# Kernel tuning notes

Measured on AMD Instinct MI355X. Metric: run time of the kernel, lower is better.

## Reference

```python
import jax, jax.numpy as jnp
import numpy as np

N, E, D, H = 50000, 800000, 128, 8
HD = D // H
EPS = 1e-5


def _layernorm(x, w, b):
    # Custom LayerNorm from the repo: divides by (unbiased std + eps), not sqrt(var+eps)
    mu = x.mean(axis=-1, keepdims=True)
    sd = x.std(axis=-1, keepdims=True, ddof=1)
    return (x - mu) / (sd + EPS) * w + b


def setup_inputs() -> dict:
    key = jax.random.key(0)
    ks = jax.random.split(key, 16)
    s = 1.0 / np.sqrt(D)
    inp = {
        "feats": jax.random.normal(ks[0], (N, D), jnp.float32),
        "edge_index": jax.random.randint(ks[1], (E, 2), 0, N, jnp.int32),
        "Wq": jax.random.normal(ks[2], (D, D), jnp.float32) * s,
        "bq": jnp.zeros((D,), jnp.float32),
        "Wk": jax.random.normal(ks[3], (D, D), jnp.float32) * s,
        "bk": jnp.zeros((D,), jnp.float32),
        "Wv": jax.random.normal(ks[4], (D, D), jnp.float32) * s,
        "bv": jnp.zeros((D,), jnp.float32),
        "Wo": jax.random.normal(ks[5], (D, D), jnp.float32) * s,
        "bo": jnp.zeros((D,), jnp.float32),
        "ln1_w": jnp.ones((D,), jnp.float32),
        "ln1_b": jnp.zeros((D,), jnp.float32),
        "ln2_w": jnp.ones((D,), jnp.float32),
        "ln2_b": jnp.zeros((D,), jnp.float32),
        "W1": jax.random.normal(ks[6], (4 * D, D), jnp.float32) * s,
        "b1": jnp.zeros((4 * D,), jnp.float32),
        "W2": jax.random.normal(ks[7], (D, 4 * D), jnp.float32) * (1.0 / np.sqrt(4 * D)),
        "b2": jnp.zeros((D,), jnp.float32),
    }
    return inp


def reference(feats, edge_index, Wq, bq, Wk, bk, Wv, bv, Wo, bo,
              ln1_w, ln1_b, ln2_w, ln2_b, W1, b1, W2, b2):
    n = feats.shape[0]
    row, col = edge_index[:, 0], edge_index[:, 1]

    # --- multi-head dot-product attention over edges (dropout = identity, eval mode) ---
    x2 = _layernorm(feats, ln1_w, ln1_b)
    q = (x2 @ Wq.T + bq).reshape(n, H, HD)
    k = (x2 @ Wk.T + bk).reshape(n, H, HD)
    v = (x2 @ Wv.T + bv).reshape(n, H, HD)

    # per-edge scores: q[col] . k[row] / sqrt(head_dim)  -> [E, H]
    scores = jnp.einsum('ehd,ehd->eh', q[col], k[row]) / np.sqrt(HD).astype(np.float32)

    # scatter softmax normalized over groups of `row`
    smax = jax.ops.segment_max(scores, row, num_segments=n)       # [N, H]
    ex = jnp.exp(scores - smax[row])                              # [E, H]
    denom = jax.ops.segment_sum(ex, row, num_segments=n)         # [N, H]
    alpha = ex / denom[row]                                       # [E, H]

    # weighted messages, aggregated at col via scatter_add
    msg = alpha[:, :, None] * v[row]                              # [E, H, HD]
    agg = jax.ops.segment_sum(msg, col, num_segments=n).reshape(n, D)
    att = agg @ Wo.T + bo

    feats = feats + att  # residual 1

    # --- MLP block: note ReLU after BOTH linears (fc_dims=[4D, D], D != 1) ---
    x2 = _layernorm(feats, ln2_w, ln2_b)
    h = jax.nn.relu(x2 @ W1.T + b1)
    h = jax.nn.relu(h @ W2.T + b2)
    feats = feats + h  # residual 2
    return feats
```

## Files before the change

### kernel.cpp

```cpp
#include <hip/hip_runtime.h>
#include <hip/hip_bf16.h>
#include <math.h>

#define H_HEADS 8
constexpr float LN_EPS = 1e-5f;
constexpr int NBCH = 64;
constexpr int NSEG = 4;

using short8 = __attribute__((ext_vector_type(8))) short;
using f32x4  = __attribute__((ext_vector_type(4))) float;
using f32x2  = __attribute__((ext_vector_type(2))) float;
using half2v = __attribute__((ext_vector_type(2))) _Float16;

#if defined(__has_builtin)
#  if __has_builtin(__builtin_amdgcn_cvt_pk_f32_fp8) && __has_builtin(__builtin_amdgcn_cvt_pk_fp8_f32)
#    define HAS_CVT_FP8 1
#  endif
#endif
#ifndef HAS_CVT_FP8
#  define HAS_CVT_FP8 0
#endif

__device__ __forceinline__ ushort f2bf(float v){
  __hip_bfloat16 h = __float2bfloat16(v);
  return *reinterpret_cast<ushort*>(&h);
}
__device__ __forceinline__ float bf2f(ushort u){
  return __uint_as_float(((unsigned)u) << 16);
}

__device__ __forceinline__ unsigned char f32_to_fp8(float v){
#if HAS_CVT_FP8
  return (unsigned char)(__builtin_amdgcn_cvt_pk_fp8_f32(v, v, 0, false) & 0xff);
#else
  _Float16 hv = (_Float16)v;
  ushort h = __builtin_bit_cast(ushort, hv);
  unsigned sign = (h >> 8) & 0x80;
  unsigned p = h & 0x7fff;
  if (p < 0x2400u) return (unsigned char)sign;
  unsigned q = (p - 0x2000u + 0x40u) >> 7;
  if (q > 0x7eu) q = 0x7eu;
  return (unsigned char)(sign | q);
#endif
}
__device__ __forceinline__ float fp8_to_f32(unsigned b){
  unsigned p = b & 0x7f;
  ushort hbits = (ushort)(((b & 0x80) << 8) | (p ? ((p << 7) + 0x2000u) : 0));
  _Float16 hv = __builtin_bit_cast(_Float16, hbits);
  return (float)hv;
}

__device__ __forceinline__ void stage16(const ushort* g, ushort* l){
  __builtin_amdgcn_global_load_lds((const __attribute__((address_space(1))) unsigned*)g,
                                   (__attribute__((address_space(3))) unsigned*)l,
                                   16, 0, 0);
}

struct CvtArgs { const float* s[6]; ushort* d[6]; int cnt[6]; };
__global__ void cvt6_kernel(CvtArgs a){
  int w = blockIdx.y;
  int i = blockIdx.x*blockDim.x + threadIdx.x;
  if (i < a.cnt[w]) a.d[w][i] = f2bf(a.s[w][i]);
}

template<int K, int RELU, int RESID, int OUTMODE>
__device__ __forceinline__ void gemm_lds_body(
    const ushort* __restrict__ A, const ushort* __restrict__ W,
    const float* __restrict__ bias, const float* __restrict__ resid,
    void* __restrict__ out, int M, int Nout, int cb, ushort* Wl){
  constexpr int NCH = K / 128;
  int t = threadIdx.x;
  int wid = t >> 6, lane = t & 63;
  int mb = blockIdx.x * 128 + wid * 16;
  int lrow = lane & 15, kgrp = lane >> 4;
  int row = mb + lrow;
  bool waveok = mb < M;
  bool rowok = row < M;
  const ushort* arow = A + (size_t)(rowok ? row : (M-1)) * K + kgrp*8;

  f32x4 acc[8] = {};
  short8 af[2][4];

  #pragma unroll
  for (int p = 0; p < 4; ++p){
    int L = p*512 + t;
    int colp = L >> 4, sp = L & 15;
    stage16(W + (size_t)colp*K + ((sp ^ (colp & 7)) << 3),
            (ushort*)((char*)Wl + ((size_t)(p*512 + (t & ~63)))*16));
  }
  if (waveok){
    #pragma unroll
    for (int kk = 0; kk < 4; ++kk)
      af[0][kk] = *(const short8*)(arow + kk*32);
  }

  #pragma unroll
  for (int ci = 0; ci < NCH; ++ci){
    __syncthreads();
    int cur = ci & 1;
    if (waveok){
      if (ci + 1 < NCH){
        #pragma unroll
        for (int kk = 0; kk < 4; ++kk)
          af[cur^1][kk] = *(const short8*)(arow + (ci+1)*128 + kk*32);
      }
      #pragma unroll
      for (int kk = 0; kk < 4; ++kk){
        #pragma unroll
        for (int nt = 0; nt < 8; ++nt){
          int colc = nt*16 + lrow;
          int g = kk*4 + kgrp;
          short8 bfv = *(const short8*)((const char*)Wl + colc*256 + ((g ^ (colc & 7))*16));
          acc[nt] = __builtin_amdgcn_mfma_f32_16x16x32_bf16(af[cur][kk], bfv, acc[nt], 0, 0, 0);
        }
      }
    }
    if (ci + 1 < NCH){
      __syncthreads();
      const ushort* Wc = W + (ci+1)*128;
      #pragma unroll
      for (int p = 0; p < 4; ++p){
        int L = p*512 + t;
        int colp = L >> 4, sp = L & 15;
        stage16(Wc + (size_t)colp*K + ((sp ^ (colp & 7)) << 3),
                (ushort*)((char*)Wl + ((size_t)(p*512 + (t & ~63)))*16));
      }
    }
  }
  if (!waveok) return;

  int r0 = mb + kgrp*4;
  #pragma unroll
  for (int nt = 0; nt < 8; ++nt){
    int c = cb + nt*16 + lrow;
    float bsum = bias[c];
    #pragma unroll
    for (int i = 0; i < 4; ++i){
      int r = r0 + i;
      if (r >= M) continue;
      float v = acc[nt][i] + bsum;
      if (RELU)  v = fmaxf(v, 0.0f);
      if (RESID) v += resid[(size_t)r*Nout + c];
      if (OUTMODE == 1) ((ushort*)out)[(size_t)r*Nout + c] = f2bf(v);
      else if (OUTMODE == 2){
        _Float16 hv = (_Float16)v;
        ((ushort*)out)[(size_t)r*Nout + c] = __builtin_bit_cast(ushort, hv);
      } else ((float*)out)[(size_t)r*Nout + c] = v;
    }
  }
}

template<int K, int RELU, int RESID, int OUTMODE>
__global__ __launch_bounds__(512) void gemm_lds(
    const ushort* __restrict__ A, const ushort* __restrict__ Wfull,
    const float* __restrict__ bias, const float* __restrict__ resid,
    void* __restrict__ out, int M, int Nout){
  __shared__ __align__(16) ushort Wl[16384];
  int cb = blockIdx.y * 128;
  gemm_lds_body<K,RELU,RESID,OUTMODE>(A, Wfull + (size_t)cb*K, bias, resid, out, M, Nout, cb, Wl);
}

__global__ __launch_bounds__(512) void qkv_fused(
    const float* __restrict__ feats, const ushort* __restrict__ Wcat,
    const float* __restrict__ ln1w, const float* __restrict__ ln1b,
    const float* __restrict__ bq, const float* __restrict__ bk, const float* __restrict__ bv,
    unsigned char* __restrict__ qb8, ushort* __restrict__ kb, ushort* __restrict__ vb, int M){
  constexpr int K = 128;
  __shared__ __align__(16) ushort Wl[16384];
  int t = threadIdx.x;
  int wid = t >> 6, lane = t & 63;
  int mb = blockIdx.x * 128 + wid * 16;
  int lrow = lane & 15, kgrp = lane >> 4;
  int row = mb + lrow;
  bool waveok = mb < M;
  bool rowok = row < M;
  int rclamp = rowok ? row : (M-1);
  const float* frow = feats + (size_t)rclamp*K + kgrp*8;

  float fx[32];
  #pragma unroll
  for (int kk = 0; kk < 4; ++kk){
    float4 a = *(const float4*)(frow + kk*32);
    float4 b = *(const float4*)(frow + kk*32 + 4);
    fx[kk*8+0]=a.x; fx[kk*8+1]=a.y; fx[kk*8+2]=a.z; fx[kk*8+3]=a.w;
    fx[kk*8+4]=b.x; fx[kk*8+5]=b.y; fx[kk*8+6]=b.z; fx[kk*8+7]=b.w;
  }
  float s = 0.f;
  #pragma unroll
  for (int i = 0; i < 32; ++i) s += fx[i];
  s += __shfl_xor(s, 16); s += __shfl_xor(s, 32);
  float mu = s * (1.0f/128.0f);
  float ss = 0.f;
  #pragma unroll
  for (int i = 0; i < 32; ++i){ fx[i] -= mu; ss += fx[i]*fx[i]; }
  ss += __shfl_xor(ss, 16); ss += __shfl_xor(ss, 32);
  float inv = 1.0f / (sqrtf(ss * (1.0f/127.0f)) + LN_EPS);

  short8 af[4];
  #pragma unroll
  for (int kk = 0; kk < 4; ++kk){
    const float* wp = ln1w + kgrp*8 + kk*32;
    const float* bp = ln1b + kgrp*8 + kk*32;
    float4 w0 = *(const float4*)wp,  w1 = *(const float4*)(wp+4);
    float4 b0 = *(const float4*)bp,  b1 = *(const float4*)(bp+4);
    float wv[8] = {w0.x,w0.y,w0.z,w0.w,w1.x,w1.y,w1.z,w1.w};
    float bvv[8]= {b0.x,b0.y,b0.z,b0.w,b1.x,b1.y,b1.z,b1.w};
    #pragma unroll
    for (int j = 0; j < 8; ++j)
      af[kk][j] = (short)f2bf(fx[kk*8+j]*inv*wv[j] + bvv[j]);
  }

  #pragma unroll
  for (int y = 0; y < 3; ++y){
    if (y) __syncthreads();
    const ushort* W = Wcat + (size_t)y*16384;
    #pragma unroll
    for (int p = 0; p < 4; ++p){
      int L = p*512 + t;
      int colp = L >> 4, sp = L & 15;
      stage16(W + (size_t)colp*K + ((sp ^ (colp & 7)) << 3),
              (ushort*)((char*)Wl + ((size_t)(p*512 + (t & ~63)))*16));
    }
    __syncthreads();
    if (waveok){
      const float* bias = (y==0) ? bq : (y==1) ? bk : bv;
      f32x4 acc[8] = {};
      #pragma unroll
      for (int kk = 0; kk < 4; ++kk){
        #pragma unroll
        for (int nt = 0; nt < 8; ++nt){
          int colc = nt*16 + lrow;
          int g = kk*4 + kgrp;
          short8 bfv = *(const short8*)((const char*)Wl + colc*256 + ((g ^ (colc & 7))*16));
          acc[nt] = __builtin_amdgcn_mfma_f32_16x16x32_bf16(af[kk], bfv, acc[nt], 0, 0, 0);
        }
      }
      int r0 = mb + kgrp*4;
      #pragma unroll
      for (int nt = 0; nt < 8; ++nt){
        int c = nt*16 + lrow;
        float bsum = bias[c];
        #pragma unroll
        for (int i = 0; i < 4; ++i){
          int r = r0 + i;
          if (r >= M) continue;
          float v = acc[nt][i] + bsum;
          if (y == 0)      qb8[(size_t)r*128 + c] = f32_to_fp8(v);
          else if (y == 1){
            _Float16 hv = (_Float16)v;
            kb[(size_t)r*128 + c] = __builtin_bit_cast(ushort, hv);
          } else           vb[(size_t)r*128 + c] = f2bf(v);
        }
      }
    }
  }
}

__global__ __launch_bounds__(512) void gemm_wo_ln2(
    const ushort* __restrict__ A, const ushort* __restrict__ W,
    const float* __restrict__ bias, const float* __restrict__ feats,
    const float* __restrict__ lnw, const float* __restrict__ lnb,
    float* __restrict__ outp, ushort* __restrict__ x2b, int M){
  constexpr int K = 128;
  __shared__ __align__(16) ushort Wl[16384];
  int t = threadIdx.x;
  int wid = t >> 6, lane = t & 63;
  int mb = blockIdx.x * 128 + wid * 16;
  int lrow = lane & 15, kgrp = lane >> 4;
  int row = mb + lrow;
  bool waveok = mb < M;
  bool rowok = row < M;
  const ushort* arow = A + (size_t)(rowok ? row : (M-1)) * K + kgrp*8;

  f32x4 acc[8] = {};
  short8 af[4];

  #pragma unroll
  for (int p = 0; p < 4; ++p){
    int L = p*512 + t;
    int colp = L >> 4, sp = L & 15;
    stage16(W + (size_t)colp*K + ((sp ^ (colp & 7)) << 3),
            (ushort*)((char*)Wl + ((size_t)(p*512 + (t & ~63)))*16));
  }
  if (waveok){
    #pragma unroll
    for (int kk = 0; kk < 4; ++kk)
      af[kk] = *(const short8*)(arow + kk*32);
  }
  __syncthreads();
  if (!waveok) return;

  #pragma unroll
  for (int kk = 0; kk < 4; ++kk){
    #pragma unroll
    for (int nt = 0; nt < 8; ++nt){
      int colc = nt*16 + lrow;
      int g = kk*4 + kgrp;
      short8 bfv = *(const short8*)((const char*)Wl + colc*256 + ((g ^ (colc & 7))*16));
      acc[nt] = __builtin_amdgcn_mfma_f32_16x16x32_bf16(af[kk], bfv, acc[nt], 0, 0, 0);
    }
  }

  int r0 = mb + kgrp*4;
  float vv[8][4];
  float lw[8], lb[8];
  #pragma unroll
  for (int nt = 0; nt < 8; ++nt){
    int c = nt*16 + lrow;
    float bsum = bias[c];
    lw[nt] = lnw[c]; lb[nt] = lnb[c];
    #pragma unroll
    for (int i = 0; i < 4; ++i){
      int r = r0 + i;
      float v = 0.f;
      if (r < M){
        v = acc[nt][i] + bsum + feats[(size_t)r*128 + c];
        outp[(size_t)r*128 + c] = v;
      }
      vv[nt][i] = v;
    }
  }
  #pragma unroll
  for (int i = 0; i < 4; ++i){
    int r = r0 + i;
    float s = 0.f;
    #pragma unroll
    for (int nt = 0; nt < 8; ++nt) s += vv[nt][i];
    #pragma unroll
    for (int o = 1; o < 16; o <<= 1) s += __shfl_xor(s, o);
    float mu = s * (1.0f/128.0f);
    float ss = 0.f;
    float d[8];
    #pragma unroll
    for (int nt = 0; nt < 8; ++nt){ d[nt] = vv[nt][i] - mu; ss += d[nt]*d[nt]; }
    #pragma unroll
    for (int o = 1; o < 16; o <<= 1) ss += __shfl_xor(ss, o);
    float sd = sqrtf(ss * (1.0f/127.0f));
    float inv = 1.0f / (sd + LN_EPS);
    if (r < M){
      #pragma unroll
      for (int nt = 0; nt < 8; ++nt){
        int c = nt*16 + lrow;
        x2b[(size_t)r*128 + c] = f2bf(d[nt]*inv*lw[nt] + lb[nt]);
      }
    }
  }
}

__global__ __launch_bounds__(256) void hist_seg2(const int* __restrict__ ei,
    unsigned* __restrict__ copies, int E, int n, int nw, int chunk, int nsb){
  __shared__ unsigned hh[12544];
  int b = blockIdx.x, s = blockIdx.y, t = threadIdx.x;
  int bin0 = s * nsb;
  int bin1 = min(bin0 + nsb, n);
  int words = (bin1 - bin0 + 1) >> 1;
  for (int i = t; i < 2*words; i += 256) hh[i] = 0;
  __syncthreads();
  int lo = b*chunk, hi = min(lo + chunk, E);
  for (int e = lo + t; e < hi; e += 256){
    int2 rc = ((const int2*)ei)[e];
    if (rc.x >= bin0 && rc.x < bin1)
      atomicAdd(&hh[(rc.x - bin0) >> 1], 1u << ((rc.x & 1)*16));
    if (rc.y >= bin0 && rc.y < bin1)
      atomicAdd(&hh[words + ((rc.y - bin0) >> 1)], 1u << ((rc.y & 1)*16));
  }
  __syncthreads();
  unsigned* d0 = copies + (size_t)b*nw + (bin0 >> 1);
  unsigned* d1 = copies + (size_t)(NBCH + b)*nw + (bin0 >> 1);
  for (int i = t; i < words; i += 256){ d0[i] = hh[i]; d1[i] = hh[words + i]; }
}

__global__ __launch_bounds__(256) void scan_fold2(const unsigned* __restrict__ copies,
    int* __restrict__ cnt2, ushort* __restrict__ choff, int* __restrict__ partial,
    int n, int nw, int npb){
  int y = blockIdx.y;
  int t = threadIdx.x;
  int bin = blockIdx.x*256 + t;
  int run = 0;
  if (bin < n){
    const unsigned* cp = copies + (size_t)y*NBCH*nw + (bin >> 1);
    int sh = (bin & 1)*16;
    for (int b = 0; b < NBCH; ++b){
      int c = (int)((cp[(size_t)b*nw] >> sh) & 0xffffu);
      choff[((size_t)y*NBCH + b)*n + bin] = (ushort)run;
      run += c;
    }
    cnt2[(size_t)y*n + bin] = run;
  }
  __shared__ int sm[256];
  sm[t] = (bin < n) ? run : 0;
  __syncthreads();
  for (int off = 128; off; off >>= 1){
    if (t < off) sm[t] += sm[t+off];
    __syncthreads();
  }
  if (t == 0) partial[y*npb + blockIdx.x] = sm[0];
}

__global__ __launch_bounds__(256) void scan_mid(int* __restrict__ partial, int nb,
                                                int* __restrict__ rptr, int* __restrict__ cptr, int n){
  int y = blockIdx.y;
  int* p = partial + y*nb;
  int t = threadIdx.x;
  __shared__ int sm[256];
  sm[t] = (t < nb) ? p[t] : 0;
  __syncthreads();
  for (int off = 1; off < 256; off <<= 1){
    int v = (t >= off) ? sm[t-off] : 0;
    __syncthreads();
    sm[t] += v;
    __syncthreads();
  }
  if (t < nb) p[t] = (t == 0) ? 0 : sm[t-1];
  if (t == 0) (y ? cptr : rptr)[n] = sm[255];
}

__global__ __launch_bounds__(256) void scan_scatter2(const int* __restrict__ cnt2,
    const int* __restrict__ partial, int* __restrict__ rptr, int* __restrict__ cptr,
    int n, int npb){
  int y = blockIdx.y;
  int* ptr = y ? cptr : rptr;
  int t = threadIdx.x;
  int bin = blockIdx.x*256 + t;
  int v = (bin < n) ? cnt2[(size_t)y*n + bin] : 0;
  __shared__ int sm[256];
  sm[t] = v;
  __syncthreads();
  for (int off = 1; off < 256; off <<= 1){
    int x = (t >= off) ? sm[t-off] : 0;
    __syncthreads();
    sm[t] += x;
    __syncthreads();
  }
  if (bin < n) ptr[bin] = partial[y*npb + blockIdx.x] + sm[t] - v;
}

__global__ __launch_bounds__(256) void fill_r_seg(const int* __restrict__ ei,
    const int* __restrict__ rptr, const ushort* __restrict__ choffR,
    int* __restrict__ rcol, int* __restrict__ pose, int E, int n, int chunk, int nsb){
  __shared__ unsigned hh[8192];
  int b = blockIdx.x, s = blockIdx.y, t = threadIdx.x;
  int bin0 = s * nsb;
  int bin1 = min(bin0 + nsb, n);
  int words = (bin1 - bin0 + 1) >> 1;
  for (int i = t; i < words; i += 256) hh[i] = 0;
  __syncthreads();
  const ushort* chb = choffR + (size_t)b*n;
  int lo = b*chunk, hi = min(lo + chunk, E);
  for (int e = lo + t; e < hi; e += 256){
    int2 rc = ((const int2*)ei)[e];
    int bin = rc.x;
    if (bin < bin0 || bin >= bin1) continue;
    int sh = (bin & 1)*16;
    unsigned old = atomicAdd(&hh[(bin - bin0) >> 1], 1u << sh);
    int rank = (int)((old >> sh) & 0xffffu);
    int pos = rptr[bin] + (int)chb[bin] + rank;
    rcol[pos] = rc.y;
    pose[e] = pos;
  }
}

__global__ __launch_bounds__(256) void fill_c_seg(const int* __restrict__ ei,
    const int* __restrict__ cptr, const ushort* __restrict__ choffC,
    const int* __restrict__ pose, int* __restrict__ crow, int* __restrict__ cposr,
    int E, int n, int chunk, int nsb){
  __shared__ unsigned hh[8192];
  int b = blockIdx.x, s = blockIdx.y, t = threadIdx.x;
  int bin0 = s * nsb;
  int bin1 = min(bin0 + nsb, n);
  int words = (bin1 - bin0 + 1) >> 1;
  for (int i = t; i < words; i += 256) hh[i] = 0;
  __syncthreads();
  const ushort* chb = choffC + (size_t)b*n;
  int lo = b*chunk, hi = min(lo + chunk, E);
  for (int e = lo + t; e < hi; e += 256){
    int2 rc = ((const int2*)ei)[e];
    int bin = rc.y;
    if (bin < bin0 || bin >= bin1) continue;
    int sh = (bin & 1)*16;
    unsigned old = atomicAdd(&hh[(bin - bin0) >> 1], 1u << sh);
    int rank = (int)((old >> sh) & 0xffffu);
    int pos = cptr[bin] + (int)chb[bin] + rank;
    crow[pos] = rc.x;
    cposr[pose[e]] = pos;
  }
}

__device__ __forceinline__ float qdot16q8(const unsigned char* __restrict__ qb8, int c, int h,
                                          const float* kf){
  const uint4* qp = (const uint4*)(qb8 + (size_t)c*128 + h*16);
  uint4 q = *qp;
  unsigned w[4] = {q.x, q.y, q.z, q.w};
  float s = 0.f;
  #pragma unroll
  for (int i = 0; i < 4; ++i){
#if HAS_CVT_FP8
    f32x2 lo = __builtin_amdgcn_cvt_pk_f32_fp8(w[i], false);
    f32x2 hi = __builtin_amdgcn_cvt_pk_f32_fp8(w[i], true);
    s = fmaf(lo[0], kf[4*i+0], s);
    s = fmaf(lo[1], kf[4*i+1], s);
    s = fmaf(hi[0], kf[4*i+2], s);
    s = fmaf(hi[1], kf[4*i+3], s);
#else
    #pragma unroll
    for (int j = 0; j < 4; ++j)
      s = fmaf(fp8_to_f32((w[i] >> (8*j)) & 0xffu), kf[4*i+j], s);
#endif
  }
  return s * 0.25f;
}

template<int NS>
__device__ __forceinline__ void softmax_rows(const unsigned char* __restrict__ qb8,
    const int* __restrict__ rcol, const int* __restrict__ cposr,
    ushort* __restrict__ cbuf, const float* kf, int lo, int hi, int h, int el,
    int rl, int cpl){
  float sreg[NS];
  float m = -1e30f;
  #pragma unroll
  for (int ts = 0; ts < NS; ++ts){
    int c = __shfl(rl, el + ts*8);
    int j = lo + el + ts*8;
    float s = -1e30f;
    if (j < hi) s = qdot16q8(qb8, c, h, kf);
    sreg[ts] = s;
    m = fmaxf(m, s);
  }
  if (NS == 8)
    for (int j = lo + el + 64; j < hi; j += 8)
      m = fmaxf(m, qdot16q8(qb8, rcol[j], h, kf));
  #pragma unroll
  for (int o = 8; o < 64; o <<= 1) m = fmaxf(m, __shfl_xor(m, o));

  float d = 0.f;
  #pragma unroll
  for (int ts = 0; ts < NS; ++ts){
    int j = lo + el + ts*8;
    if (j < hi){ float e = __expf(sreg[ts] - m); sreg[ts] = e; d += e; }
  }
  if (NS == 8)
    for (int j = lo + el + 64; j < hi; j += 8)
      d += __expf(qdot16q8(qb8, rcol[j], h, kf) - m);
  #pragma unroll
  for (int o = 8; o < 64; o <<= 1) d += __shfl_xor(d, o);
  float invd = 1.0f / d;

  #pragma unroll
  for (int ts = 0; ts < NS; ++ts){
    int cp = __shfl(cpl, el + ts*8);
    int j = lo + el + ts*8;
    if (j < hi) cbuf[(size_t)cp*8 + h] = f2bf(sreg[ts] * invd);
  }
  if (NS == 8)
    for (int j = lo + el + 64; j < hi; j += 8){
      float s = qdot16q8(qb8, rcol[j], h, kf);
      cbuf[(size_t)cposr[j]*8 + h] = f2bf(__expf(s - m) * invd);
    }
}

__global__ void row_softmax_kernel(const unsigned char* __restrict__ qb8,
                                   const ushort* __restrict__ kb,
                                   const int* __restrict__ rptr, const int* __restrict__ rcol,
                                   const int* __restrict__ cposr,
                                   ushort* __restrict__ cbuf, int n){
  int wid = threadIdx.x >> 6, lane = threadIdx.x & 63;
  int r = blockIdx.x * (blockDim.x >> 6) + wid;
  if (r >= n) return;
  int lo = rptr[r], hi = rptr[r+1];
  if (lo >= hi) return;
  int h = lane & 7, el = lane >> 3;

  int jl = lo + lane;
  bool jok = jl < hi;
  int rl  = rcol [jok ? jl : lo];
  int cpl = cposr[jok ? jl : lo];

  float kf[16];
  {
    const int4* kp = (const int4*)(kb + (size_t)r*128 + h*16);
    int4 k0 = kp[0], k1 = kp[1];
    int kw[8] = {k0.x,k0.y,k0.z,k0.w,k1.x,k1.y,k1.z,k1.w};
    #pragma unroll
    for (int i = 0; i < 8; ++i){
      half2v k2 = __builtin_bit_cast(half2v, kw[i]);
      kf[2*i]   = (float)k2.x;
      kf[2*i+1] = (float)k2.y;
    }
  }

  int deg = hi - lo;
  if (deg <= 16)      softmax_rows<2>(qb8, rcol, cposr, cbuf, kf, lo, hi, h, el, rl, cpl);
  else if (deg <= 32) softmax_rows<4>(qb8, rcol, cposr, cbuf, kf, lo, hi, h, el, rl, cpl);
  else                softmax_rows<8>(qb8, rcol, cposr, cbuf, kf, lo, hi, h, el, rl, cpl);
}

__global__ void agg_kernel(const ushort* __restrict__ vb, const ushort* __restrict__ cbuf,
                           const int* __restrict__ cptr, const int* __restrict__ crow,
                           ushort* __restrict__ aggb, int n){
  int wid = threadIdx.x >> 6, lane = threadIdx.x & 63;
  int node = blockIdx.x * (blockDim.x >> 6) + wid;
  if (node >= n) return;
  int lo = cptr[node], hi = cptr[node+1];
  int deg = hi - lo;
  int oct = lane >> 3, l8 = lane & 7;

  int jl = lo + lane;
  int crl = crow[jl < hi ? jl : lo];

  float acc[16] = {};
  int tmax = (deg + 7) >> 3;
  for (int ts = 0; ts < tmax; ++ts){
    int li = oct + ts*8;
    int row = __shfl(crl, li & 63);
    if (li < deg){
      if (li >= 64) row = crow[lo + li];
      float a = bf2f(cbuf[(size_t)(lo + li)*8 + l8]);
      const short8* vp = (const short8*)(vb + (size_t)row*128 + l8*16);
      short8 v0 = vp[0], v1 = vp[1];
      #pragma unroll
      for (int i = 0; i < 8; ++i){
        acc[i]   = fmaf(a, bf2f((ushort)v0[i]), acc[i]);
        acc[8+i] = fmaf(a, bf2f((ushort)v1[i]), acc[8+i]);
      }
    }
  }
  #pragma unroll
  for (int i = 0; i < 16; ++i){
    acc[i] += __shfl_xor(acc[i], 8);
    acc[i] += __shfl_xor(acc[i], 16);
    acc[i] += __shfl_xor(acc[i], 32);
  }
  if (oct == 0){
    short8 o0, o1;
    #pragma unroll
    for (int i = 0; i < 8; ++i){ o0[i] = (short)f2bf(acc[i]); o1[i] = (short)f2bf(acc[8+i]); }
    short8* op = (short8*)(aggb + (size_t)node*128 + l8*16);
    op[0] = o0; op[1] = o1;
  }
}

extern "C" void kernel_launch(void* const* d_in, const int* in_sizes, int n_in,
                              void* d_out, int out_size, void* d_ws, size_t ws_size,
                              hipStream_t stream){
  const float* feats = (const float*)d_in[0];
  const int*   ei    = (const int*)  d_in[1];
  const float* Wq = (const float*)d_in[2];
  const float* bq = (const float*)d_in[3];
  const float* Wk = (const float*)d_in[4];
  const float* bk = (const float*)d_in[5];
  const float* Wv = (const float*)d_in[6];
  const float* bv = (const float*)d_in[7];
  const float* Wo = (const float*)d_in[8];
  const float* bo = (const float*)d_in[9];
  const float* ln1w = (const float*)d_in[10];
  const float* ln1b = (const float*)d_in[11];
  const float* ln2w = (const float*)d_in[12];
  const float* ln2b = (const float*)d_in[13];
  const float* W1 = (const float*)d_in[14];
  const float* b1 = (const float*)d_in[15];
  const float* W2 = (const float*)d_in[16];
  const float* b2 = (const float*)d_in[17];
  float* outp = (float*)d_out;

  int n = in_sizes[0] / 128;
  int E = in_sizes[1] / 2;
  int nw = (n + 1) >> 1;
  int chunk = (E + NBCH - 1) / NBCH;
  int nsb = (((n + NSEG - 1) / NSEG) + 1) & ~1;
  int npb = (n + 255) / 256;

  const size_t ND  = (size_t)n * 128;
  const size_t ND2 = ND / 2;
  const size_t EH  = (size_t)E * H_HEADS;

  float* ws = (float*)d_ws;
  ushort* x2b  = (ushort*)ws;
  unsigned char* qb8 = (unsigned char*)(ws + ND2);
  ushort* kb   = (ushort*)(ws + 2*ND2);
  ushort* vb   = (ushort*)(ws + 3*ND2);
  ushort* cbuf = (ushort*)(ws + 4*ND2);
  ushort* aggb = (ushort*)(ws + 4*ND2 + EH/2);
  int* crow    = (int*)(ws + 5*ND2 + EH/2);
  int* cposr   = crow + E;
  int* rcol    = cposr + E;
  int* pose    = rcol + E;
  int* rptr    = pose + E;
  int* cptr    = rptr + (n + 4);
  int* cnt2    = cptr + (n + 4);
  ushort* choff = (ushort*)(cnt2 + 2*n);
  unsigned* copies = (unsigned*)(choff + (size_t)2*NBCH*n);
  int* partial = (int*)(copies + (size_t)2*NBCH*nw);
  ushort* wbuf = (ushort*)(partial + 512);
  ushort* Wqb = wbuf;
  ushort* Wkb = Wqb + 16384;
  ushort* Wvb = Wkb + 16384;
  ushort* Wob = Wvb + 16384;
  ushort* W1b = Wob + 16384;
  ushort* W2b = W1b + 65536;
  ushort* h1  = (ushort*)qb8;

  CvtArgs ca;
  ca.s[0]=Wq; ca.s[1]=Wk; ca.s[2]=Wv; ca.s[3]=Wo; ca.s[4]=W1; ca.s[5]=W2;
  ca.d[0]=Wqb; ca.d[1]=Wkb; ca.d[2]=Wvb; ca.d[3]=Wob; ca.d[4]=W1b; ca.d[5]=W2b;
  ca.cnt[0]=ca.cnt[1]=ca.cnt[2]=ca.cnt[3]=16384; ca.cnt[4]=ca.cnt[5]=65536;
  cvt6_kernel<<<dim3(65536/256, 6), 256, 0, stream>>>(ca);

  hist_seg2   <<<dim3(NBCH,NSEG), 256, 0, stream>>>(ei, copies, E, n, nw, chunk, nsb);
  scan_fold2  <<<dim3(npb,2), 256, 0, stream>>>(copies, cnt2, choff, partial, n, nw, npb);
  scan_mid    <<<dim3(1,2),   256, 0, stream>>>(partial, npb, rptr, cptr, n);
  scan_scatter2<<<dim3(npb,2),256, 0, stream>>>(cnt2, partial, rptr, cptr, n, npb);
  fill_r_seg<<<dim3(NBCH,NSEG), 256, 0, stream>>>(ei, rptr, choff,                  rcol, pose, E, n, chunk, nsb);
  fill_c_seg<<<dim3(NBCH,NSEG), 256, 0, stream>>>(ei, cptr, choff + (size_t)NBCH*n, pose, crow, cposr, E, n, chunk, nsb);

  int gm = (n + 127)/128;
  qkv_fused<<<gm, 512, 0, stream>>>(feats, Wqb, ln1w, ln1b, bq, bk, bv, qb8, kb, vb, n);

  row_softmax_kernel<<<(n+3)/4, 256, 0, stream>>>(qb8, kb, rptr, rcol, cposr, cbuf, n);

  agg_kernel<<<(n+3)/4, 256, 0, stream>>>(vb, cbuf, cptr, crow, aggb, n);

  gemm_wo_ln2<<<gm, 512, 0, stream>>>(aggb, Wob, bo, feats, ln2w, ln2b, outp, x2b, n);

  gemm_lds<128,1,0,1><<<dim3(gm,4), 512, 0, stream>>>(x2b, W1b, b1, nullptr, h1,  n, 512);
  gemm_lds<512,1,1,0><<<dim3(gm,1), 512, 0, stream>>>(h1,  W2b, b2, outp,    outp, n, 128);
}
```

Measured before the change: 265.9 us.

## Fuse FFN up and down projections into one kernel keeping hidden in LDS

Replaces the two FFN GEMM launches with a single kernel. Each block computes a 128-column chunk of the ReLU hidden activation, stores it in swizzled LDS as bf16, and immediately accumulates it into the second GEMM against the matching W2 slice. This removes the global write and read of the N×512 hidden tensor and one kernel launch. In exchange it uses twice the LDS per block, adds more barriers with no overlap between weight staging and MFMA work, and has fewer blocks in flight (gm instead of gm×4 for the first GEMM).

```diff
diff --git a/kernel.cpp b/kernel.cpp
--- a/kernel.cpp
+++ b/kernel.cpp
@@ -61,103 +61,6 @@
   int w = blockIdx.y;
   int i = blockIdx.x*blockDim.x + threadIdx.x;
   if (i < a.cnt[w]) a.d[w][i] = f2bf(a.s[w][i]);
-}
-
-template<int K, int RELU, int RESID, int OUTMODE>
-__device__ __forceinline__ void gemm_lds_body(
-    const ushort* __restrict__ A, const ushort* __restrict__ W,
-    const float* __restrict__ bias, const float* __restrict__ resid,
-    void* __restrict__ out, int M, int Nout, int cb, ushort* Wl){
-  constexpr int NCH = K / 128;
-  int t = threadIdx.x;
-  int wid = t >> 6, lane = t & 63;
-  int mb = blockIdx.x * 128 + wid * 16;
-  int lrow = lane & 15, kgrp = lane >> 4;
-  int row = mb + lrow;
-  bool waveok = mb < M;
-  bool rowok = row < M;
-  const ushort* arow = A + (size_t)(rowok ? row : (M-1)) * K + kgrp*8;
-
-  f32x4 acc[8] = {};
-  short8 af[2][4];
-
-  #pragma unroll
-  for (int p = 0; p < 4; ++p){
-    int L = p*512 + t;
-    int colp = L >> 4, sp = L & 15;
-    stage16(W + (size_t)colp*K + ((sp ^ (colp & 7)) << 3),
-            (ushort*)((char*)Wl + ((size_t)(p*512 + (t & ~63)))*16));
-  }
-  if (waveok){
-    #pragma unroll
-    for (int kk = 0; kk < 4; ++kk)
-      af[0][kk] = *(const short8*)(arow + kk*32);
-  }
-
-  #pragma unroll
-  for (int ci = 0; ci < NCH; ++ci){
-    __syncthreads();
-    int cur = ci & 1;
-    if (waveok){
-      if (ci + 1 < NCH){
-        #pragma unroll
-        for (int kk = 0; kk < 4; ++kk)
-          af[cur^1][kk] = *(const short8*)(arow + (ci+1)*128 + kk*32);
-      }
-      #pragma unroll
-      for (int kk = 0; kk < 4; ++kk){
-        #pragma unroll
-        for (int nt = 0; nt < 8; ++nt){
-          int colc = nt*16 + lrow;
-          int g = kk*4 + kgrp;
-          short8 bfv = *(const short8*)((const char*)Wl + colc*256 + ((g ^ (colc & 7))*16));
-          acc[nt] = __builtin_amdgcn_mfma_f32_16x16x32_bf16(af[cur][kk], bfv, acc[nt], 0, 0, 0);
-        }
-      }
-    }
-    if (ci + 1 < NCH){
-      __syncthreads();
-      const ushort* Wc = W + (ci+1)*128;
-      #pragma unroll
-      for (int p = 0; p < 4; ++p){
-        int L = p*512 + t;
-        int colp = L >> 4, sp = L & 15;
-        stage16(Wc + (size_t)colp*K + ((sp ^ (colp & 7)) << 3),
-                (ushort*)((char*)Wl + ((size_t)(p*512 + (t & ~63)))*16));
-      }
-    }
-  }
-  if (!waveok) return;
-
-  int r0 = mb + kgrp*4;
-  #pragma unroll
-  for (int nt = 0; nt < 8; ++nt){
-    int c = cb + nt*16 + lrow;
-    float bsum = bias[c];
-    #pragma unroll
-    for (int i = 0; i < 4; ++i){
-      int r = r0 + i;
-      if (r >= M) continue;
-      float v = acc[nt][i] + bsum;
-      if (RELU)  v = fmaxf(v, 0.0f);
-      if (RESID) v += resid[(size_t)r*Nout + c];
-      if (OUTMODE == 1) ((ushort*)out)[(size_t)r*Nout + c] = f2bf(v);
-      else if (OUTMODE == 2){
-        _Float16 hv = (_Float16)v;
-        ((ushort*)out)[(size_t)r*Nout + c] = __builtin_bit_cast(ushort, hv);
-      } else ((float*)out)[(size_t)r*Nout + c] = v;
-    }
-  }
-}
-
-template<int K, int RELU, int RESID, int OUTMODE>
-__global__ __launch_bounds__(512) void gemm_lds(
-    const ushort* __restrict__ A, const ushort* __restrict__ Wfull,
-    const float* __restrict__ bias, const float* __restrict__ resid,
-    void* __restrict__ out, int M, int Nout){
-  __shared__ __align__(16) ushort Wl[16384];
-  int cb = blockIdx.y * 128;
-  gemm_lds_body<K,RELU,RESID,OUTMODE>(A, Wfull + (size_t)cb*K, bias, resid, out, M, Nout, cb, Wl);
 }
 
 __global__ __launch_bounds__(512) void qkv_fused(
@@ -343,6 +246,112 @@
         int c = nt*16 + lrow;
         x2b[(size_t)r*128 + c] = f2bf(d[nt]*inv*lw[nt] + lb[nt]);
       }
+    }
+  }
+}
+
+__global__ __launch_bounds__(512) void gemm_ffn(
+    const ushort* __restrict__ x2b, const ushort* __restrict__ W1b,
+    const ushort* __restrict__ W2b, const float* __restrict__ b1,
+    const float* __restrict__ b2, float* __restrict__ outp, int M){
+  __shared__ __align__(16) ushort Wl[16384];
+  __shared__ __align__(16) ushort Hl[16384];
+  int t = threadIdx.x;
+  int wid = t >> 6, lane = t & 63;
+  int mb = blockIdx.x * 128 + wid * 16;
+  int lrow = lane & 15, kgrp = lane >> 4;
+  int row = mb + lrow;
+  bool waveok = mb < M;
+  bool rowok = row < M;
+  const ushort* arow = x2b + (size_t)(rowok ? row : (M-1))*128 + kgrp*8;
+
+  short8 af[4];
+  if (waveok){
+    #pragma unroll
+    for (int kk = 0; kk < 4; ++kk)
+      af[kk] = *(const short8*)(arow + kk*32);
+  }
+
+  f32x4 acc2[8] = {};
+  int lr = wid*16 + lrow;
+  int r0 = mb + kgrp*4;
+
+  #pragma unroll
+  for (int kc = 0; kc < 4; ++kc){
+    const ushort* W1c = W1b + (size_t)kc*128*128;
+    #pragma unroll
+    for (int p = 0; p < 4; ++p){
+      int L = p*512 + t;
+      int colp = L >> 4, sp = L & 15;
+      stage16(W1c + (size_t)colp*128 + ((sp ^ (colp & 7)) << 3),
+              (ushort*)((char*)Wl + ((size_t)(p*512 + (t & ~63)))*16));
+    }
+    __syncthreads();
+    if (waveok){
+      f32x4 acc1[8] = {};
+      #pragma unroll
+      for (int kk = 0; kk < 4; ++kk){
+        #pragma unroll
+        for (int nt = 0; nt < 8; ++nt){
+          int colc = nt*16 + lrow;
+          int g = kk*4 + kgrp;
+          short8 bfv = *(const short8*)((const char*)Wl + colc*256 + ((g ^ (colc & 7))*16));
+          acc1[nt] = __builtin_amdgcn_mfma_f32_16x16x32_bf16(af[kk], bfv, acc1[nt], 0, 0, 0);
+        }
+      }
+      #pragma unroll
+      for (int nt = 0; nt < 8; ++nt){
+        int c = nt*16 + lrow;
+        float bsum = b1[kc*128 + c];
+        #pragma unroll
+        for (int i = 0; i < 4; ++i){
+          int R = wid*16 + kgrp*4 + i;
+          float v = fmaxf(acc1[nt][i] + bsum, 0.0f);
+          *(ushort*)((char*)Hl + R*256 + (((c >> 3) ^ (R & 7)) << 4) + (c & 7)*2) = f2bf(v);
+        }
+      }
+    }
+    __syncthreads();
+    #pragma unroll
+    for (int p = 0; p < 4; ++p){
+      int L = p*512 + t;
+      int colp = L >> 4, sp = L & 15;
+      stage16(W2b + (size_t)colp*512 + kc*128 + ((sp ^ (colp & 7)) << 3),
+              (ushort*)((char*)Wl + ((size_t)(p*512 + (t & ~63)))*16));
+    }
+    __syncthreads();
+    if (waveok){
+      short8 ah[4];
+      #pragma unroll
+      for (int kk = 0; kk < 4; ++kk){
+        int g = kk*4 + kgrp;
+        ah[kk] = *(const short8*)((const char*)Hl + lr*256 + ((g ^ (lr & 7)) << 4));
+      }
+      #pragma unroll
+      for (int kk = 0; kk < 4; ++kk){
+        #pragma unroll
+        for (int nt = 0; nt < 8; ++nt){
+          int colc = nt*16 + lrow;
+          int g = kk*4 + kgrp;
+          short8 bfv = *(const short8*)((const char*)Wl + colc*256 + ((g ^ (colc & 7))*16));
+          acc2[nt] = __builtin_amdgcn_mfma_f32_16x16x32_bf16(ah[kk], bfv, acc2[nt], 0, 0, 0);
+        }
+      }
+    }
+    __syncthreads();
+  }
+  if (!waveok) return;
+
+  #pragma unroll
+  for (int nt = 0; nt < 8; ++nt){
+    int c = nt*16 + lrow;
+    float bsum = b2[c];
+    #pragma unroll
+    for (int i = 0; i < 4; ++i){
+      int r = r0 + i;
+      if (r >= M) continue;
+      float v = fmaxf(acc2[nt][i] + bsum, 0.0f) + outp[(size_t)r*128 + c];
+      outp[(size_t)r*128 + c] = v;
     }
   }
 }
@@ -697,7 +706,6 @@
   ushort* Wob = Wvb + 16384;
   ushort* W1b = Wob + 16384;
   ushort* W2b = W1b + 65536;
-  ushort* h1  = (ushort*)qb8;
 
   CvtArgs ca;
   ca.s[0]=Wq; ca.s[1]=Wk; ca.s[2]=Wv; ca.s[3]=Wo; ca.s[4]=W1; ca.s[5]=W2;
@@ -721,6 +729,5 @@
 
   gemm_wo_ln2<<<gm, 512, 0, stream>>>(aggb, Wob, bo, feats, ln2w, ln2b, outp, x2b, n);
 
-  gemm_lds<128,1,0,1><<<dim3(gm,4), 512, 0, stream>>>(x2b, W1b, b1, nullptr, h1,  n, 512);
-  gemm_lds<512,1,1,0><<<dim3(gm,1), 512, 0, stream>>>(h1,  W2b, b2, outp,    outp, n, 128);
-}
+  gemm_ffn<<<gm, 512, 0, stream>>>(x2b, W1b, W2b, b1, b2, outp, n);
+}
```

Measured after the change: 273.8 us. 1.03x slower.
